# Performance work log

Hardware: AMD Instinct MI355X
Metric: run time of the kernel (lower is better)

The kernel has to match this reference:

```python
import jax, jax.numpy as jnp
import numpy as np
import math

SPAN = 50  # hardcoded attn_span in the module


def _xavier(k, shape):
    limit = math.sqrt(6.0 / (shape[0] + shape[1]))
    return jax.random.uniform(k, shape, jnp.float32, -limit, limit)


def setup_inputs() -> dict:
    k0 = jax.random.key(0)
    ks = jax.random.split(k0, 12)
    n, E, H = 4096, 128, 8
    return {
        "query": jax.random.normal(ks[0], (n, E), jnp.float32),
        "key": jax.random.normal(ks[1], (n, E), jnp.float32),
        "value": jax.random.normal(ks[2], (n, E), jnp.float32),
        "attn_bias": jax.random.normal(ks[3], (n, H), jnp.float32),
        "Wq": _xavier(ks[4], (E, E)), "bq": jnp.zeros((E,), jnp.float32),
        "Wk": _xavier(ks[5], (E, E)), "bk": jnp.zeros((E,), jnp.float32),
        "Wv": _xavier(ks[6], (E, E)), "bv": jnp.zeros((E,), jnp.float32),
        "Wo": _xavier(ks[7], (E, E)), "bo": jnp.zeros((E,), jnp.float32),
        "Wfe": _xavier(ks[8], (H, E)), "bfe": jnp.zeros((E,), jnp.float32),
    }


def reference(query, key, value, attn_bias, Wq, bq, Wk, bk, Wv, bv, Wo, bo, Wfe, bfe):
    n, E = query.shape
    H = attn_bias.shape[1]
    d = E // H
    W = 2 * SPAN + 1

    q = (query @ Wq + bq).reshape(n, H, d)
    k = (key @ Wk + bk).reshape(n, H, d)
    v = (value @ Wv + bv).reshape(n, H, d)
    b = (attn_bias @ Wfe + bfe).reshape(n, H, d)

    offsets = jnp.arange(-SPAN, SPAN + 1)              # (W,)
    cols = jnp.arange(n)[:, None] + offsets[None, :]   # (n, W)
    bounds = (cols >= 0) & (cols < n)
    cols_c = jnp.where(bounds, cols, 0)

    k_g = k[cols_c]  # (n, W, H, d)
    v_g = v[cols_c]
    b_g = b[cols_c]

    scale = 1.0 / math.sqrt(n)  # original divides by sqrt(n)
    scores = jnp.einsum('nhd,nwhd->nhw', q, k_g) * scale
    scores = scores + jnp.einsum('nhd,nwhd->nhw', b, b_g)
    scores = jnp.where(bounds[:, None, :], scores, -jnp.inf)

    probs = jax.nn.softmax(scores, axis=-1)            # (n, H, W)
    out = jnp.einsum('nhw,nwhd->nhd', probs, v_g).reshape(n, E)
    return out @ Wo + bo
```

## Files before the change

### kernel.cpp

```cpp
#include <hip/hip_runtime.h>
#include <math.h>

constexpr int N = 4096;
constexpr int E = 128;
constexpr int H = 8;
constexpr int D = 16;
constexpr int SPAN = 50;

__device__ __forceinline__ void gemm_fma4(const float4 x, const float4 w0,
                                          const float4 w1, const float4 w2,
                                          const float4 w3, float4& a)
{
    a.x = fmaf(x.x, w0.x, a.x); a.y = fmaf(x.x, w0.y, a.y);
    a.z = fmaf(x.x, w0.z, a.z); a.w = fmaf(x.x, w0.w, a.w);
    a.x = fmaf(x.y, w1.x, a.x); a.y = fmaf(x.y, w1.y, a.y);
    a.z = fmaf(x.y, w1.z, a.z); a.w = fmaf(x.y, w1.w, a.w);
    a.x = fmaf(x.z, w2.x, a.x); a.y = fmaf(x.z, w2.y, a.y);
    a.z = fmaf(x.z, w2.z, a.z); a.w = fmaf(x.z, w2.w, a.w);
    a.x = fmaf(x.w, w3.x, a.x); a.y = fmaf(x.w, w3.y, a.y);
    a.z = fmaf(x.w, w3.z, a.z); a.w = fmaf(x.w, w3.w, a.w);
}

__global__ __launch_bounds__(256) void proj_kernel(
    const float* __restrict__ query, const float* __restrict__ key,
    const float* __restrict__ value, const float* __restrict__ attn_bias,
    const float* __restrict__ Wq, const float* __restrict__ bq,
    const float* __restrict__ Wk, const float* __restrict__ bk,
    const float* __restrict__ Wv, const float* __restrict__ bv,
    const float* __restrict__ Wfe, const float* __restrict__ bfe,
    float* __restrict__ qo, float* __restrict__ ko,
    float* __restrict__ vo, float* __restrict__ bo_)
{
    __shared__ __align__(16) float xs[16 * 128];
    __shared__ __align__(16) float ab[16 * 8];
    __shared__ __align__(16) float part[2 * 16 * 132];

    const int tid  = threadIdx.x;
    const int c4   = tid & 31;
    const int rg   = (tid >> 5) & 3;
    const int kh   = tid >> 7;
    const int bid  = blockIdx.x;
    const int mat  = bid >> 8;
    const int row0 = (bid & 255) * 16;

    const float* src  = mat == 0 ? query : (mat == 1 ? key : value);
    const float* Wm   = mat == 0 ? Wq : (mat == 1 ? Wk : Wv);
    const float* bias = mat == 0 ? bq : (mat == 1 ? bk : bv);
    float*       dst  = mat == 0 ? qo : (mat == 1 ? ko : vo);

    #pragma unroll
    for (int rr = 0; rr < 2; ++rr) {
        const int idx = tid + 256 * rr;
        const int row = idx >> 5, q = idx & 31;
        *(float4*)&xs[row * 128 + q * 4] =
            ((const float4*)(src + (size_t)(row0 + row) * E))[q];
    }
    if (mat == 0 && tid < 128) ab[tid] = attn_bias[(size_t)row0 * H + tid];
    __syncthreads();

    const int kb = kh * 64;
    {
        float4 acc[4];
        #pragma unroll
        for (int i = 0; i < 4; ++i) acc[i] = make_float4(0.f, 0.f, 0.f, 0.f);

        #pragma unroll 2
        for (int kk = 0; kk < 64; kk += 4) {
            const int k = kb + kk;
            const float4 w0 = ((const float4*)(Wm + (size_t)(k + 0) * E))[c4];
            const float4 w1 = ((const float4*)(Wm + (size_t)(k + 1) * E))[c4];
            const float4 w2 = ((const float4*)(Wm + (size_t)(k + 2) * E))[c4];
            const float4 w3 = ((const float4*)(Wm + (size_t)(k + 3) * E))[c4];
            const float4 x0 = *(const float4*)&xs[(rg +  0) * 128 + k];
            const float4 x1 = *(const float4*)&xs[(rg +  4) * 128 + k];
            const float4 x2 = *(const float4*)&xs[(rg +  8) * 128 + k];
            const float4 x3 = *(const float4*)&xs[(rg + 12) * 128 + k];
            gemm_fma4(x0, w0, w1, w2, w3, acc[0]);
            gemm_fma4(x1, w0, w1, w2, w3, acc[1]);
            gemm_fma4(x2, w0, w1, w2, w3, acc[2]);
            gemm_fma4(x3, w0, w1, w2, w3, acc[3]);
        }
        #pragma unroll
        for (int i = 0; i < 4; ++i)
            *(float4*)&part[(size_t)(kh * 16 + rg + 4 * i) * 132 + c4 * 4] = acc[i];
        __syncthreads();
        #pragma unroll
        for (int u = 0; u < 2; ++u) {
            const int o = tid + 256 * u;
            const int row = o >> 5, q = o & 31;
            const float4 p0 = *(const float4*)&part[(size_t)row * 132 + q * 4];
            const float4 p1 = *(const float4*)&part[(size_t)(16 + row) * 132 + q * 4];
            const float4 bb = ((const float4*)bias)[q];
            *(float4*)(dst + (size_t)(row0 + row) * E + q * 4) =
                make_float4(p0.x + p1.x + bb.x, p0.y + p1.y + bb.y,
                            p0.z + p1.z + bb.z, p0.w + p1.w + bb.w);
        }
    }

    if (mat == 0) {
        __syncthreads();
        float4 acc[4];
        #pragma unroll
        for (int i = 0; i < 4; ++i) acc[i] = make_float4(0.f, 0.f, 0.f, 0.f);
        const float4 w0 = ((const float4*)(Wfe + (size_t)(kh * 4 + 0) * E))[c4];
        const float4 w1 = ((const float4*)(Wfe + (size_t)(kh * 4 + 1) * E))[c4];
        const float4 w2 = ((const float4*)(Wfe + (size_t)(kh * 4 + 2) * E))[c4];
        const float4 w3 = ((const float4*)(Wfe + (size_t)(kh * 4 + 3) * E))[c4];
        #pragma unroll
        for (int i = 0; i < 4; ++i) {
            const float4 x = *(const float4*)&ab[(rg + 4 * i) * 8 + kh * 4];
            gemm_fma4(x, w0, w1, w2, w3, acc[i]);
        }
        #pragma unroll
        for (int i = 0; i < 4; ++i)
            *(float4*)&part[(size_t)(kh * 16 + rg + 4 * i) * 132 + c4 * 4] = acc[i];
        __syncthreads();
        #pragma unroll
        for (int u = 0; u < 2; ++u) {
            const int o = tid + 256 * u;
            const int row = o >> 5, q = o & 31;
            const float4 p0 = *(const float4*)&part[(size_t)row * 132 + q * 4];
            const float4 p1 = *(const float4*)&part[(size_t)(16 + row) * 132 + q * 4];
            const float4 bb = ((const float4*)bfe)[q];
            *(float4*)(bo_ + (size_t)(row0 + row) * E + q * 4) =
                make_float4(p0.x + p1.x + bb.x, p0.y + p1.y + bb.y,
                            p0.z + p1.z + bb.z, p0.w + p1.w + bb.w);
        }
    }
}

__global__ __launch_bounds__(512, 4) void attn_out_kernel(
    const float* __restrict__ qw, const float* __restrict__ kw,
    const float* __restrict__ vw, const float* __restrict__ bw,
    const float* __restrict__ Wo, const float* __restrict__ bop,
    float* __restrict__ out)
{
    __shared__ __align__(16) float vt[8][2176];
    __shared__ float ewb[8][104];
    __shared__ float at[8 * 132];

    const int tid  = threadIdx.x;
    const int lane = tid & 63;
    const int h    = __builtin_amdgcn_readfirstlane(tid >> 6);
    const int bid  = blockIdx.x;
    const int swz  = ((bid & 7) << 6) | (bid >> 3);
    const int i0   = swz * 8;
    const int base = i0 - SPAN;

    float* vtw = &vt[h][0];
    float* eww = &ewb[h][0];

    {
        const int x4 = lane & 3, rr = lane >> 2;
        #pragma unroll
        for (int rep = 0; rep < 8; ++rep) {
            const int r = rep * 16 + rr;
            int j = base + r;
            j = j < 0 ? 0 : (j > N - 1 ? N - 1 : j);
            const float4 t = *(const float4*)(vw + (size_t)j * E + h * D + x4 * 4);
            vtw[r * 17 + x4 * 4 + 0] = t.x; vtw[r * 17 + x4 * 4 + 1] = t.y;
            vtw[r * 17 + x4 * 4 + 2] = t.z; vtw[r * 17 + x4 * 4 + 3] = t.w;
        }
    }

    const int p0 = base + lane;
    const int p1 = p0 + 64;
    const bool in0 = (p0 >= 0) && (p0 < N);
    const bool in1 = (p1 < N);
    const int c0 = p0 < 0 ? 0 : (p0 > N - 1 ? N - 1 : p0);
    const int c1 = p1 > N - 1 ? N - 1 : p1;

    float k0[16], k1[16], g0[16], g1[16];
    {
        const float4* kp0 = (const float4*)(kw + (size_t)c0 * E + h * D);
        const float4* kp1 = (const float4*)(kw + (size_t)c1 * E + h * D);
        const float4* gp0 = (const float4*)(bw + (size_t)c0 * E + h * D);
        const float4* gp1 = (const float4*)(bw + (size_t)c1 * E + h * D);
        #pragma unroll
        for (int x = 0; x < 4; ++x) {
            float4 t;
            t = kp0[x]; k0[4*x]=t.x; k0[4*x+1]=t.y; k0[4*x+2]=t.z; k0[4*x+3]=t.w;
            t = kp1[x]; k1[4*x]=t.x; k1[4*x+1]=t.y; k1[4*x+2]=t.z; k1[4*x+3]=t.w;
            t = gp0[x]; g0[4*x]=t.x; g0[4*x+1]=t.y; g0[4*x+2]=t.z; g0[4*x+3]=t.w;
            t = gp1[x]; g1[4*x]=t.x; g1[4*x+1]=t.y; g1[4*x+2]=t.z; g1[4*x+3]=t.w;
        }
    }

    const float scale = 1.0f / 64.0f;
    const int d = lane & 15;
    const int g = lane >> 4;

    for (int r = 0; r < 8; ++r) {
        const float* qp = qw + (size_t)(i0 + r) * E + h * D;
        const float* bp = bw + (size_t)(i0 + r) * E + h * D;

        float sq0 = 0.f, sq1 = 0.f, sb0 = 0.f, sb1 = 0.f;
        #pragma unroll
        for (int x = 0; x < 16; ++x) {
            const float qv = qp[x];
            const float bv = bp[x];
            sq0 = fmaf(qv, k0[x], sq0);
            sq1 = fmaf(qv, k1[x], sq1);
            sb0 = fmaf(bv, g0[x], sb0);
            sb1 = fmaf(bv, g1[x], sb1);
        }
        const bool ok0 = in0 && (lane >= r);
        const bool ok1 = in1 && (lane <= r + 36);
        const float e0 = ok0 ? __expf(sq0 * scale + sb0) : 0.f;
        const float e1 = ok1 ? __expf(sq1 * scale + sb1) : 0.f;

        if (lane >= r)      eww[lane - r]      = e0;
        if (lane <= r + 36) eww[64 + lane - r] = e1;

        float acc = 0.f, as = 0.f;
        #pragma unroll
        for (int it = 0; it < 25; ++it) {
            const int w = g + 4 * it;
            const float p = eww[w];
            acc = fmaf(p, vtw[(w + r) * 17 + d], acc);
            as += p;
        }
        if (g == 0) {
            const float p = eww[100];
            acc = fmaf(p, vtw[(100 + r) * 17 + d], acc);
            as += p;
        }
        acc += __shfl_xor(acc, 16); as += __shfl_xor(as, 16);
        acc += __shfl_xor(acc, 32); as += __shfl_xor(as, 32);
        if (lane < D) at[r * 132 + h * D + lane] = acc / as;
    }

    __syncthreads();

    {
        float* part = &vt[0][0];
        const int wh  = tid >> 8;
        const int idx = tid & 255;
        const int c4  = idx & 31;
        const int row = idx >> 5;
        const int kb  = wh * 64;

        float4 acc = make_float4(0.f, 0.f, 0.f, 0.f);
        #pragma unroll 2
        for (int kk = 0; kk < 64; kk += 4) {
            const int k = kb + kk;
            const float4 w0 = ((const float4*)(Wo + (size_t)(k + 0) * E))[c4];
            const float4 w1 = ((const float4*)(Wo + (size_t)(k + 1) * E))[c4];
            const float4 w2 = ((const float4*)(Wo + (size_t)(k + 2) * E))[c4];
            const float4 w3 = ((const float4*)(Wo + (size_t)(k + 3) * E))[c4];
            const float4 x  = *(const float4*)&at[row * 132 + k];
            gemm_fma4(x, w0, w1, w2, w3, acc);
        }
        *(float4*)&part[(size_t)(wh * 8 + row) * 132 + c4 * 4] = acc;
        __syncthreads();

        if (tid < 256) {
            const int orow = tid >> 5, q = tid & 31;
            const float4 p0 = *(const float4*)&part[(size_t)orow * 132 + q * 4];
            const float4 p1 = *(const float4*)&part[(size_t)(8 + orow) * 132 + q * 4];
            const float4 bb = ((const float4*)bop)[q];
            *(float4*)(out + (size_t)(i0 + orow) * E + q * 4) =
                make_float4(p0.x + p1.x + bb.x, p0.y + p1.y + bb.y,
                            p0.z + p1.z + bb.z, p0.w + p1.w + bb.w);
        }
    }
}

extern "C" void kernel_launch(void* const* d_in, const int* in_sizes, int n_in,
                              void* d_out, int out_size, void* d_ws, size_t ws_size,
                              hipStream_t stream) {
    const float* query     = (const float*)d_in[0];
    const float* key       = (const float*)d_in[1];
    const float* value     = (const float*)d_in[2];
    const float* attn_bias = (const float*)d_in[3];
    const float* Wq  = (const float*)d_in[4];
    const float* bq  = (const float*)d_in[5];
    const float* Wk  = (const float*)d_in[6];
    const float* bk  = (const float*)d_in[7];
    const float* Wv  = (const float*)d_in[8];
    const float* bv  = (const float*)d_in[9];
    const float* Wo  = (const float*)d_in[10];
    const float* bo  = (const float*)d_in[11];
    const float* Wfe = (const float*)d_in[12];
    const float* bfe = (const float*)d_in[13];

    float* ws = (float*)d_ws;
    const int NE = N * E;
    float* qw = ws;
    float* kw = ws + 1 * NE;
    float* vw = ws + 2 * NE;
    float* bw = ws + 3 * NE;

    proj_kernel<<<3 * 256, 256, 0, stream>>>(query, key, value, attn_bias,
                                             Wq, bq, Wk, bk, Wv, bv,
                                             Wfe, bfe, qw, kw, vw, bw);
    attn_out_kernel<<<N / 8, 512, 0, stream>>>(qw, kw, vw, bw, Wo, bo,
                                               (float*)d_out);
}
```

Measured before the change: 40.82 us.

## Split each head's attention window across two wavefronts with 1024-thread blocks

Doubles the block to 1024 threads so each head uses two wavefronts, each owning one half of the 101-wide window. Each wave holds one key/bias row instead of two, which cuts register pressure, and partial numerators and denominators are combined through shared memory before normalisation. The output projection is split four ways along K to use the extra threads. The cost is an extra shared-memory reduction stage, extra barriers, and a large block whose occupancy depends on register and LDS use.

```diff
diff --git a/kernel.cpp b/kernel.cpp
--- a/kernel.cpp
+++ b/kernel.cpp
@@ -129,32 +129,36 @@
     }
 }
 
-__global__ __launch_bounds__(512, 4) void attn_out_kernel(
+__global__ __launch_bounds__(1024, 4) void attn_out_kernel(
     const float* __restrict__ qw, const float* __restrict__ kw,
     const float* __restrict__ vw, const float* __restrict__ bw,
     const float* __restrict__ Wo, const float* __restrict__ bop,
     float* __restrict__ out)
 {
-    __shared__ __align__(16) float vt[8][2176];
-    __shared__ float ewb[8][104];
-    __shared__ float at[8 * 132];
+    __shared__ __align__(16) float vt[8][112 * 17];
+    __shared__ float ew0[8][64];
+    __shared__ float ew1[8][52];
+    __shared__ float pacc[8][2][8][17];
 
     const int tid  = threadIdx.x;
     const int lane = tid & 63;
-    const int h    = __builtin_amdgcn_readfirstlane(tid >> 6);
+    const int wid  = tid >> 6;
+    const int h    = __builtin_amdgcn_readfirstlane(wid >> 1);
+    const int half = __builtin_amdgcn_readfirstlane(wid & 1);
     const int bid  = blockIdx.x;
     const int swz  = ((bid & 7) << 6) | (bid >> 3);
     const int i0   = swz * 8;
     const int base = i0 - SPAN;
 
     float* vtw = &vt[h][0];
-    float* eww = &ewb[h][0];
+
+    if (half == 1 && lane < 7) ew1[h][45 + lane] = 0.f;
 
     {
         const int x4 = lane & 3, rr = lane >> 2;
-        #pragma unroll
-        for (int rep = 0; rep < 8; ++rep) {
-            const int r = rep * 16 + rr;
+        const int nrep = half == 0 ? 4 : 3;
+        for (int rep = 0; rep < nrep; ++rep) {
+            const int r = half * 64 + rep * 16 + rr;
             int j = base + r;
             j = j < 0 ? 0 : (j > N - 1 ? N - 1 : j);
             const float4 t = *(const float4*)(vw + (size_t)j * E + h * D + x4 * 4);
@@ -163,28 +167,23 @@
         }
     }
 
-    const int p0 = base + lane;
-    const int p1 = p0 + 64;
-    const bool in0 = (p0 >= 0) && (p0 < N);
-    const bool in1 = (p1 < N);
-    const int c0 = p0 < 0 ? 0 : (p0 > N - 1 ? N - 1 : p0);
-    const int c1 = p1 > N - 1 ? N - 1 : p1;
-
-    float k0[16], k1[16], g0[16], g1[16];
-    {
-        const float4* kp0 = (const float4*)(kw + (size_t)c0 * E + h * D);
-        const float4* kp1 = (const float4*)(kw + (size_t)c1 * E + h * D);
-        const float4* gp0 = (const float4*)(bw + (size_t)c0 * E + h * D);
-        const float4* gp1 = (const float4*)(bw + (size_t)c1 * E + h * D);
+    const int p   = base + half * 64 + lane;
+    const bool inb = (p >= 0) && (p < N);
+    const int cp  = p < 0 ? 0 : (p > N - 1 ? N - 1 : p);
+
+    float kr[16], gr[16];
+    {
+        const float4* kp = (const float4*)(kw + (size_t)cp * E + h * D);
+        const float4* gp = (const float4*)(bw + (size_t)cp * E + h * D);
         #pragma unroll
         for (int x = 0; x < 4; ++x) {
             float4 t;
-            t = kp0[x]; k0[4*x]=t.x; k0[4*x+1]=t.y; k0[4*x+2]=t.z; k0[4*x+3]=t.w;
-            t = kp1[x]; k1[4*x]=t.x; k1[4*x+1]=t.y; k1[4*x+2]=t.z; k1[4*x+3]=t.w;
-            t = gp0[x]; g0[4*x]=t.x; g0[4*x+1]=t.y; g0[4*x+2]=t.z; g0[4*x+3]=t.w;
-            t = gp1[x]; g1[4*x]=t.x; g1[4*x+1]=t.y; g1[4*x+2]=t.z; g1[4*x+3]=t.w;
-        }
-    }
+            t = kp[x]; kr[4*x]=t.x; kr[4*x+1]=t.y; kr[4*x+2]=t.z; kr[4*x+3]=t.w;
+            t = gp[x]; gr[4*x]=t.x; gr[4*x+1]=t.y; gr[4*x+2]=t.z; gr[4*x+3]=t.w;
+        }
+    }
+
+    __syncthreads();
 
     const float scale = 1.0f / 64.0f;
     const int d = lane & 15;
@@ -194,55 +193,68 @@
         const float* qp = qw + (size_t)(i0 + r) * E + h * D;
         const float* bp = bw + (size_t)(i0 + r) * E + h * D;
 
-        float sq0 = 0.f, sq1 = 0.f, sb0 = 0.f, sb1 = 0.f;
+        float sq = 0.f, sb = 0.f;
         #pragma unroll
         for (int x = 0; x < 16; ++x) {
-            const float qv = qp[x];
-            const float bv = bp[x];
-            sq0 = fmaf(qv, k0[x], sq0);
-            sq1 = fmaf(qv, k1[x], sq1);
-            sb0 = fmaf(bv, g0[x], sb0);
-            sb1 = fmaf(bv, g1[x], sb1);
-        }
-        const bool ok0 = in0 && (lane >= r);
-        const bool ok1 = in1 && (lane <= r + 36);
-        const float e0 = ok0 ? __expf(sq0 * scale + sb0) : 0.f;
-        const float e1 = ok1 ? __expf(sq1 * scale + sb1) : 0.f;
-
-        if (lane >= r)      eww[lane - r]      = e0;
-        if (lane <= r + 36) eww[64 + lane - r] = e1;
-
-        float acc = 0.f, as = 0.f;
-        #pragma unroll
-        for (int it = 0; it < 25; ++it) {
-            const int w = g + 4 * it;
-            const float p = eww[w];
-            acc = fmaf(p, vtw[(w + r) * 17 + d], acc);
-            as += p;
-        }
-        if (g == 0) {
-            const float p = eww[100];
-            acc = fmaf(p, vtw[(100 + r) * 17 + d], acc);
-            as += p;
-        }
-        acc += __shfl_xor(acc, 16); as += __shfl_xor(as, 16);
-        acc += __shfl_xor(acc, 32); as += __shfl_xor(as, 32);
-        if (lane < D) at[r * 132 + h * D + lane] = acc / as;
+            sq = fmaf(qp[x], kr[x], sq);
+            sb = fmaf(bp[x], gr[x], sb);
+        }
+        const int wc = half * 64 + lane - r;
+        const bool valid = inb && ((unsigned)wc <= 100u);
+        const float e = valid ? __expf(sq * scale + sb) : 0.f;
+        if ((unsigned)wc <= 100u) {
+            if (half == 0) ew0[h][wc] = e;
+            else           ew1[h][wc - 56] = e;
+        }
+
+        float acc = 0.f, sum = 0.f;
+        if (half == 0) {
+            const int wlim = 63 - r;
+            #pragma unroll
+            for (int it = 0; it < 16; ++it) {
+                const int w = g + 4 * it;
+                const float pv = (w <= wlim) ? ew0[h][w] : 0.f;
+                acc = fmaf(pv, vtw[(w + r) * 17 + d], acc);
+                sum += pv;
+            }
+        } else {
+            const int wbase = 64 - r + g;
+            #pragma unroll
+            for (int it = 0; it < 11; ++it) {
+                const int w = wbase + 4 * it;
+                const float pv = ew1[h][w - 56];
+                acc = fmaf(pv, vtw[(w + r) * 17 + d], acc);
+                sum += pv;
+            }
+        }
+        acc += __shfl_xor(acc, 16); sum += __shfl_xor(sum, 16);
+        acc += __shfl_xor(acc, 32); sum += __shfl_xor(sum, 32);
+        if (lane < 16) pacc[h][half][r][lane] = acc;
+        if (lane == 0) pacc[h][half][r][16]  = sum;
     }
 
     __syncthreads();
 
-    {
-        float* part = &vt[0][0];
+    float* at = &vt[0][0];
+    {
+        const int h2 = tid >> 7, r2 = (tid >> 4) & 7, d2 = tid & 15;
+        const float a = pacc[h2][0][r2][d2] + pacc[h2][1][r2][d2];
+        const float s = pacc[h2][0][r2][16] + pacc[h2][1][r2][16];
+        at[r2 * 132 + h2 * 16 + d2] = a / s;
+    }
+    __syncthreads();
+
+    {
+        float* part = &vt[0][0] + 4224;
         const int wh  = tid >> 8;
         const int idx = tid & 255;
         const int c4  = idx & 31;
         const int row = idx >> 5;
-        const int kb  = wh * 64;
+        const int kb  = wh * 32;
 
         float4 acc = make_float4(0.f, 0.f, 0.f, 0.f);
         #pragma unroll 2
-        for (int kk = 0; kk < 64; kk += 4) {
+        for (int kk = 0; kk < 32; kk += 4) {
             const int k = kb + kk;
             const float4 w0 = ((const float4*)(Wo + (size_t)(k + 0) * E))[c4];
             const float4 w1 = ((const float4*)(Wo + (size_t)(k + 1) * E))[c4];
@@ -256,12 +268,16 @@
 
         if (tid < 256) {
             const int orow = tid >> 5, q = tid & 31;
-            const float4 p0 = *(const float4*)&part[(size_t)orow * 132 + q * 4];
-            const float4 p1 = *(const float4*)&part[(size_t)(8 + orow) * 132 + q * 4];
+            const float4 p0 = *(const float4*)&part[(size_t)(orow     ) * 132 + q * 4];
+            const float4 p1 = *(const float4*)&part[(size_t)(orow +  8) * 132 + q * 4];
+            const float4 p2 = *(const float4*)&part[(size_t)(orow + 16) * 132 + q * 4];
+            const float4 p3 = *(const float4*)&part[(size_t)(orow + 24) * 132 + q * 4];
             const float4 bb = ((const float4*)bop)[q];
             *(float4*)(out + (size_t)(i0 + orow) * E + q * 4) =
-                make_float4(p0.x + p1.x + bb.x, p0.y + p1.y + bb.y,
-                            p0.z + p1.z + bb.z, p0.w + p1.w + bb.w);
+                make_float4(p0.x + p1.x + p2.x + p3.x + bb.x,
+                            p0.y + p1.y + p2.y + p3.y + bb.y,
+                            p0.z + p1.z + p2.z + p3.z + bb.z,
+                            p0.w + p1.w + p2.w + p3.w + bb.w);
         }
     }
 }
@@ -294,6 +310,6 @@
     proj_kernel<<<3 * 256, 256, 0, stream>>>(query, key, value, attn_bias,
                                              Wq, bq, Wk, bk, Wv, bv,
                                              Wfe, bfe, qw, kw, vw, bw);
-    attn_out_kernel<<<N / 8, 512, 0, stream>>>(qw, kw, vw, bw, Wo, bo,
-                                               (float*)d_out);
+    attn_out_kernel<<<N / 8, 1024, 0, stream>>>(qw, kw, vw, bw, Wo, bo,
+                                                (float*)d_out);
 }
```

After: 50.55 us. +23.8%, slower.
